# Optimization experiments

Hardware: AMD Instinct MI355X
Metric: run time of the kernel (lower is better)

## Reference

```python
import jax, jax.numpy as jnp
import numpy as np

B, IN, OUT, G = 16, 1024, 1024, 8  # G = grid_size + spline_order = 5 + 3

def setup_inputs() -> dict:
    key = jax.random.key(0)
    k1, k2, k3 = jax.random.split(key, 3)
    x = jax.random.normal(k1, (B, IN), dtype=jnp.float32)
    # kaiming-uniform-ish init for base_weight, normal(0, 0.1) for grid
    bound = 1.0 / np.sqrt(IN)
    base_weight = jax.random.uniform(k2, (OUT, IN), dtype=jnp.float32, minval=-bound, maxval=bound)
    grid = 0.1 * jax.random.normal(k3, (IN, OUT, G), dtype=jnp.float32)
    return {"x": x, "base_weight": base_weight, "grid": grid}

def reference(x, base_weight, grid):
    # base: [B, OUT] = x @ W^T
    base_output = jnp.einsum("bi,oi->bo", x, base_weight)
    # spline basis: sigmoid(x[b,i] + grid[i,o,g]) -> [B, IN, OUT, G], reduced over i and g
    spline_basis = jax.nn.sigmoid(x[:, :, None, None] + grid[None, :, :, :])
    spline_output = jnp.sum(spline_basis, axis=(1, 3))  # [B, OUT]
    return base_output + spline_output
```

## Files before the change

### kernel.cpp

```cpp
#include <hip/hip_runtime.h>

#define B_ 16
#define IN_ 1024
#define OUT_ 1024
#define G_ 8
#define OTILE 64
#define ITILE 32
#define NOT_ (OUT_/OTILE)
#define NIT_ (IN_/ITILE)

__device__ __forceinline__ float rcp_f(float x) { return __builtin_amdgcn_rcpf(x); }

__global__ __launch_bounds__(256, 2) void kan_main(
    const float* __restrict__ x,
    const float* __restrict__ W,
    const float* __restrict__ gridp,
    float* __restrict__ out)
{
    __shared__ float xs[B_][ITILE];
    __shared__ float es[B_][ITILE];
    __shared__ float red[4][B_][OTILE];

    const int tid  = threadIdx.x;
    const int ot   = blockIdx.x & (NOT_-1);
    const int it   = blockIdx.x / NOT_;
    const int i0   = it * ITILE;
    const int lane = tid & 63;
    const int q    = tid >> 6;
    const int o    = ot * OTILE + lane;

    const float NL2E = -1.44269504088896340736f;

    for (int k = tid; k < B_*ITILE; k += 256) {
        const int b  = k >> 5;
        const int il = k & 31;
        const float xv = x[b*IN_ + i0 + il];
        xs[b][il] = xv;
        es[b][il] = exp2f(NL2E * xv);
    }
    __syncthreads();

    float acc[B_];
    #pragma unroll
    for (int b = 0; b < B_; ++b) acc[b] = 0.0f;

    const int ibase = i0 + q * 8;
    const float* gp = gridp + (size_t)ibase * (OUT_*G_) + (size_t)o * G_;
    const float* wp = W + (size_t)o * IN_ + ibase;

    float4 w0 = *(const float4*)(wp);
    float4 w1 = *(const float4*)(wp + 4);
    float wv[8] = {w0.x, w0.y, w0.z, w0.w, w1.x, w1.y, w1.z, w1.w};

    for (int ii = 0; ii < 8; ++ii) {
        const int il = q*8 + ii;
        float4 ga = *(const float4*)(gp + (size_t)ii * (OUT_*G_));
        float4 gb = *(const float4*)(gp + (size_t)ii * (OUT_*G_) + 4);
        const float F0 = exp2f(NL2E * ga.x);
        const float F1 = exp2f(NL2E * ga.y);
        const float F2 = exp2f(NL2E * ga.z);
        const float F3 = exp2f(NL2E * ga.w);
        const float F4 = exp2f(NL2E * gb.x);
        const float F5 = exp2f(NL2E * gb.y);
        const float F6 = exp2f(NL2E * gb.z);
        const float F7 = exp2f(NL2E * gb.w);
        const float S0 = F0 + F1, P0 = F0 * F1;
        const float S1 = F2 + F3, P1 = F2 * F3;
        const float S2 = F4 + F5, P2 = F4 * F5;
        const float S3 = F6 + F7, P3 = F6 * F7;
        const float wvi = wv[ii];
        #pragma unroll
        for (int b = 0; b < B_; ++b) {
            const float e  = es[b][il];
            const float xv = xs[b][il];
            const float e2 = e * e;
            float t0 = fmaf(e, S0, 1.0f), n0 = t0 + 1.0f, d0 = fmaf(e2, P0, t0);
            float t1 = fmaf(e, S1, 1.0f), n1 = t1 + 1.0f, d1 = fmaf(e2, P1, t1);
            float t2 = fmaf(e, S2, 1.0f), n2 = t2 + 1.0f, d2 = fmaf(e2, P2, t2);
            float t3 = fmaf(e, S3, 1.0f), n3 = t3 + 1.0f, d3 = fmaf(e2, P3, t3);
            float na = fmaf(n0, d1, n1 * d0);
            float da = d0 * d1;
            float nb = fmaf(n2, d3, n3 * d2);
            float db = d2 * d3;
            float s  = fmaf(na, rcp_f(da), nb * rcp_f(db));
            acc[b] += fmaf(xv, wvi, s);
        }
    }

    #pragma unroll
    for (int b = 0; b < B_; ++b) red[q][b][lane] = acc[b];
    __syncthreads();
    for (int k = tid; k < B_*OTILE; k += 256) {
        const int b  = k >> 6;
        const int ol = k & 63;
        const float v = red[0][b][ol] + red[1][b][ol] + red[2][b][ol] + red[3][b][ol];
        atomicAdd(out + b*OUT_ + ot*OTILE + ol, v);
    }
}

extern "C" void kernel_launch(void* const* d_in, const int* in_sizes, int n_in,
                              void* d_out, int out_size, void* d_ws, size_t ws_size,
                              hipStream_t stream) {
    const float* x  = (const float*)d_in[0];
    const float* W  = (const float*)d_in[1];
    const float* gp = (const float*)d_in[2];
    float* out = (float*)d_out;

    hipMemsetAsync(out, 0, (size_t)B_ * OUT_ * sizeof(float), stream);
    kan_main<<<dim3(NOT_ * NIT_), dim3(256), 0, stream>>>(x, W, gp, out);
}
```

Before: 91.15 us.

## Use single rational polynomial for 8-term sigmoid sum and two-stage reduction

Rewrites the sum of eight sigmoids as one rational function of e=exp(-x). The numerator and denominator polynomial coefficients are precomputed per (i,o), so each batch element costs about 14 FMAs and one reciprocal instead of four reciprocals plus assorted FMAs. It also shrinks the input tile to 8, which quadruples the block count and raises the occupancy hint. Atomics plus the memset are replaced by per-tile partial writes to workspace and a second reduction kernel. The trade-offs are a 128-way partial buffer (8 MB of extra traffic), an extra launch, and possible loss of precision from high-degree polynomial evaluation.

```diff
diff --git a/kernel.cpp b/kernel.cpp
--- a/kernel.cpp
+++ b/kernel.cpp
@@ -5,25 +5,25 @@
 #define OUT_ 1024
 #define G_ 8
 #define OTILE 64
-#define ITILE 32
+#define ITILE 8
 #define NOT_ (OUT_/OTILE)
 #define NIT_ (IN_/ITILE)
 
-__device__ __forceinline__ float rcp_f(float x) { return __builtin_amdgcn_rcpf(x); }
+__device__ __forceinline__ float rcp_f(float x)  { return __builtin_amdgcn_rcpf(x); }
+__device__ __forceinline__ float exp2_f(float x) { return __builtin_amdgcn_exp2f(x); }
 
-__global__ __launch_bounds__(256, 2) void kan_main(
+__global__ __launch_bounds__(256, 4) void kan_stage1(
     const float* __restrict__ x,
     const float* __restrict__ W,
     const float* __restrict__ gridp,
-    float* __restrict__ out)
+    float* __restrict__ partial)
 {
-    __shared__ float xs[B_][ITILE];
-    __shared__ float es[B_][ITILE];
-    __shared__ float red[4][B_][OTILE];
+    __shared__ float2 xe[B_][ITILE];
+    __shared__ float  red[4][B_][OTILE];
 
     const int tid  = threadIdx.x;
     const int ot   = blockIdx.x & (NOT_-1);
-    const int it   = blockIdx.x / NOT_;
+    const int it   = blockIdx.x >> 4;
     const int i0   = it * ITILE;
     const int lane = tid & 63;
     const int q    = tid >> 6;
@@ -31,12 +31,11 @@
 
     const float NL2E = -1.44269504088896340736f;
 
-    for (int k = tid; k < B_*ITILE; k += 256) {
-        const int b  = k >> 5;
-        const int il = k & 31;
+    if (tid < B_*ITILE) {
+        const int b  = tid >> 3;
+        const int il = tid & 7;
         const float xv = x[b*IN_ + i0 + il];
-        xs[b][il] = xv;
-        es[b][il] = exp2f(NL2E * xv);
+        xe[b][il] = make_float2(xv, exp2_f(NL2E * xv));
     }
     __syncthreads();
 
@@ -44,58 +43,81 @@
     #pragma unroll
     for (int b = 0; b < B_; ++b) acc[b] = 0.0f;
 
-    const int ibase = i0 + q * 8;
-    const float* gp = gridp + (size_t)ibase * (OUT_*G_) + (size_t)o * G_;
-    const float* wp = W + (size_t)o * IN_ + ibase;
+    const int ib = q * 2;
+    const float* gp = gridp + (size_t)(i0 + ib) * (OUT_*G_) + (size_t)o * G_;
+    const float2 wv = *(const float2*)(W + (size_t)o * IN_ + i0 + ib);
 
-    float4 w0 = *(const float4*)(wp);
-    float4 w1 = *(const float4*)(wp + 4);
-    float wv[8] = {w0.x, w0.y, w0.z, w0.w, w1.x, w1.y, w1.z, w1.w};
+    #pragma unroll
+    for (int ii = 0; ii < 2; ++ii) {
+        const float4 ga = *(const float4*)(gp + (size_t)ii * (OUT_*G_));
+        const float4 gb = *(const float4*)(gp + (size_t)ii * (OUT_*G_) + 4);
+        const float F0 = exp2_f(NL2E * ga.x);
+        const float F1 = exp2_f(NL2E * ga.y);
+        const float F2 = exp2_f(NL2E * ga.z);
+        const float F3 = exp2_f(NL2E * ga.w);
+        const float F4 = exp2_f(NL2E * gb.x);
+        const float F5 = exp2_f(NL2E * gb.y);
+        const float F6 = exp2_f(NL2E * gb.z);
+        const float F7 = exp2_f(NL2E * gb.w);
 
-    for (int ii = 0; ii < 8; ++ii) {
-        const int il = q*8 + ii;
-        float4 ga = *(const float4*)(gp + (size_t)ii * (OUT_*G_));
-        float4 gb = *(const float4*)(gp + (size_t)ii * (OUT_*G_) + 4);
-        const float F0 = exp2f(NL2E * ga.x);
-        const float F1 = exp2f(NL2E * ga.y);
-        const float F2 = exp2f(NL2E * ga.z);
-        const float F3 = exp2f(NL2E * ga.w);
-        const float F4 = exp2f(NL2E * gb.x);
-        const float F5 = exp2f(NL2E * gb.y);
-        const float F6 = exp2f(NL2E * gb.z);
-        const float F7 = exp2f(NL2E * gb.w);
-        const float S0 = F0 + F1, P0 = F0 * F1;
-        const float S1 = F2 + F3, P1 = F2 * F3;
-        const float S2 = F4 + F5, P2 = F4 * F5;
-        const float S3 = F6 + F7, P3 = F6 * F7;
-        const float wvi = wv[ii];
+        float c1 = F0 + F1, c2 = F0 * F1, c3, c4, c5, c6, c7, c8;
+        c3 = F2*c2; c2 = fmaf(F2,c1,c2); c1 += F2;
+        c4 = F3*c3; c3 = fmaf(F3,c2,c3); c2 = fmaf(F3,c1,c2); c1 += F3;
+        c5 = F4*c4; c4 = fmaf(F4,c3,c4); c3 = fmaf(F4,c2,c3); c2 = fmaf(F4,c1,c2); c1 += F4;
+        c6 = F5*c5; c5 = fmaf(F5,c4,c5); c4 = fmaf(F5,c3,c4); c3 = fmaf(F5,c2,c3); c2 = fmaf(F5,c1,c2); c1 += F5;
+        c7 = F6*c6; c6 = fmaf(F6,c5,c6); c5 = fmaf(F6,c4,c5); c4 = fmaf(F6,c3,c4); c3 = fmaf(F6,c2,c3); c2 = fmaf(F6,c1,c2); c1 += F6;
+        c8 = F7*c7; c7 = fmaf(F7,c6,c7); c6 = fmaf(F7,c5,c6); c5 = fmaf(F7,c4,c5); c4 = fmaf(F7,c3,c4); c3 = fmaf(F7,c2,c3); c2 = fmaf(F7,c1,c2); c1 += F7;
+
+        const float t1 = 7.0f*c1, t2 = 6.0f*c2, t3 = 5.0f*c3,
+                    t4 = 4.0f*c4, t5 = 3.0f*c5, t6 = 2.0f*c6;
+
+        const float wvi = ii ? wv.y : wv.x;
+        const int   il  = ib + ii;
+
         #pragma unroll
         for (int b = 0; b < B_; ++b) {
-            const float e  = es[b][il];
-            const float xv = xs[b][il];
-            const float e2 = e * e;
-            float t0 = fmaf(e, S0, 1.0f), n0 = t0 + 1.0f, d0 = fmaf(e2, P0, t0);
-            float t1 = fmaf(e, S1, 1.0f), n1 = t1 + 1.0f, d1 = fmaf(e2, P1, t1);
-            float t2 = fmaf(e, S2, 1.0f), n2 = t2 + 1.0f, d2 = fmaf(e2, P2, t2);
-            float t3 = fmaf(e, S3, 1.0f), n3 = t3 + 1.0f, d3 = fmaf(e2, P3, t3);
-            float na = fmaf(n0, d1, n1 * d0);
-            float da = d0 * d1;
-            float nb = fmaf(n2, d3, n3 * d2);
-            float db = d2 * d3;
-            float s  = fmaf(na, rcp_f(da), nb * rcp_f(db));
-            acc[b] += fmaf(xv, wvi, s);
+            const float2 p = xe[b][il];
+            const float  e = p.y, xv = p.x;
+            float den = fmaf(c8, e, c7);
+            den = fmaf(den, e, c6); den = fmaf(den, e, c5);
+            den = fmaf(den, e, c4); den = fmaf(den, e, c3);
+            den = fmaf(den, e, c2); den = fmaf(den, e, c1);
+            den = fmaf(den, e, 1.0f);
+            float num = fmaf(c7, e, t6);
+            num = fmaf(num, e, t5); num = fmaf(num, e, t4);
+            num = fmaf(num, e, t3); num = fmaf(num, e, t2);
+            num = fmaf(num, e, t1); num = fmaf(num, e, 8.0f);
+
+            acc[b] = fmaf(num, rcp_f(den), acc[b]);
+            acc[b] = fmaf(xv, wvi, acc[b]);
         }
     }
 
     #pragma unroll
     for (int b = 0; b < B_; ++b) red[q][b][lane] = acc[b];
     __syncthreads();
+    float* pout = partial + (size_t)it * (B_*OUT_);
     for (int k = tid; k < B_*OTILE; k += 256) {
         const int b  = k >> 6;
         const int ol = k & 63;
-        const float v = red[0][b][ol] + red[1][b][ol] + red[2][b][ol] + red[3][b][ol];
-        atomicAdd(out + b*OUT_ + ot*OTILE + ol, v);
+        pout[b*OUT_ + ot*OTILE + ol] =
+            red[0][b][ol] + red[1][b][ol] + red[2][b][ol] + red[3][b][ol];
     }
+}
+
+__global__ __launch_bounds__(256) void kan_stage2(
+    const float* __restrict__ partial, float* __restrict__ out)
+{
+    const int m = blockIdx.x * 256 + threadIdx.x;
+    float s0 = 0.f, s1 = 0.f, s2 = 0.f, s3 = 0.f;
+    #pragma unroll 8
+    for (int it = 0; it < NIT_; it += 4) {
+        s0 += partial[(size_t)(it  ) * (B_*OUT_) + m];
+        s1 += partial[(size_t)(it+1) * (B_*OUT_) + m];
+        s2 += partial[(size_t)(it+2) * (B_*OUT_) + m];
+        s3 += partial[(size_t)(it+3) * (B_*OUT_) + m];
+    }
+    out[m] = (s0 + s1) + (s2 + s3);
 }
 
 extern "C" void kernel_launch(void* const* d_in, const int* in_sizes, int n_in,
@@ -104,8 +126,9 @@
     const float* x  = (const float*)d_in[0];
     const float* W  = (const float*)d_in[1];
     const float* gp = (const float*)d_in[2];
-    float* out = (float*)d_out;
+    float* out     = (float*)d_out;
+    float* partial = (float*)d_ws;
 
-    hipMemsetAsync(out, 0, (size_t)B_ * OUT_ * sizeof(float), stream);
-    kan_main<<<dim3(NOT_ * NIT_), dim3(256), 0, stream>>>(x, W, gp, out);
+    kan_stage1<<<dim3(NOT_ * NIT_), dim3(256), 0, stream>>>(x, W, gp, partial);
+    kan_stage2<<<dim3(B_ * OUT_ / 256), dim3(256), 0, stream>>>(partial, out);
 }
```

Measured after the change: 96.56 us. +5.9%, slower.
